# Kernel tuning notes

Hardware: AMD Instinct MI355X
Metric: run time of the kernel (lower is better)

## Reference

```python
import jax, jax.numpy as jnp
import numpy as np

N_SHAPE = 100
PARENTS = [-1, 0, 1, 1, 1]  # FLAME kintree: global, neck, jaw, eyeL, eyeR
NUM_JOINTS = 5


def batch_rodrigues(rot_vecs):
    # rot_vecs: [B, J, 3] axis-angle -> [B, J, 3, 3] rotation matrices
    angle = jnp.linalg.norm(rot_vecs + 1e-8, axis=-1, keepdims=True)  # [B,J,1]
    rot_dir = rot_vecs / angle
    cos = jnp.cos(angle)[..., None]  # [B,J,1,1]
    sin = jnp.sin(angle)[..., None]
    rx, ry, rz = rot_dir[..., 0], rot_dir[..., 1], rot_dir[..., 2]
    zeros = jnp.zeros_like(rx)
    K = jnp.stack([zeros, -rz, ry, rz, zeros, -rx, -ry, rx, zeros], axis=-1)
    K = K.reshape(rot_vecs.shape[:-1] + (3, 3))
    ident = jnp.eye(3, dtype=rot_vecs.dtype)
    return ident + sin * K + (1.0 - cos) * jnp.matmul(K, K)


def batch_rigid_transform(rot_mats, joints):
    # rot_mats: [B,J,3,3], joints: [B,J,3] -> relative transforms A: [B,J,4,4]
    B = rot_mats.shape[0]
    dtype = rot_mats.dtype
    parent_idx = jnp.array(PARENTS[1:])
    rel_joints = jnp.concatenate(
        [joints[:, :1], joints[:, 1:] - joints[:, parent_idx]], axis=1)
    # build local 4x4 transforms
    top = jnp.concatenate([rot_mats, rel_joints[..., None]], axis=-1)  # [B,J,3,4]
    bottom = jnp.broadcast_to(
        jnp.array([0.0, 0.0, 0.0, 1.0], dtype=dtype), (B, NUM_JOINTS, 1, 4))
    transforms_mat = jnp.concatenate([top, bottom], axis=-2)  # [B,J,4,4]
    # sequential FK chain over the (small, fixed) joint tree
    chain = [transforms_mat[:, 0]]
    for i in range(1, NUM_JOINTS):
        chain.append(jnp.matmul(chain[PARENTS[i]], transforms_mat[:, i]))
    transforms = jnp.stack(chain, axis=1)  # [B,J,4,4]
    # remove rest-pose joint location contribution
    joints_h = jnp.concatenate(
        [joints, jnp.zeros((B, NUM_JOINTS, 1), dtype=dtype)], axis=-1)  # [B,J,4]
    tj = jnp.matmul(transforms, joints_h[..., None])  # [B,J,4,1]
    rel_transforms = transforms - jnp.pad(tj, ((0, 0), (0, 0), (0, 0), (3, 0)))
    return rel_transforms


def _flame_forward(expression_params, full_pose, v_template, shapedirs,
                   posedirs, J_regressor, lbs_weights):
    B = expression_params.shape[0]
    V = v_template.shape[0]
    dtype = expression_params.dtype
    # betas = [zeros(n_shape) | expression]
    betas = jnp.concatenate(
        [jnp.zeros((B, N_SHAPE), dtype=dtype), expression_params], axis=1)
    # shape blendshapes
    v_shaped = v_template[None] + jnp.einsum('bl,vkl->bvk', betas, shapedirs)
    joints = jnp.einsum('jv,bvk->bjk', J_regressor, v_shaped)  # [B,J,3]
    # pose -> rotation matrices, pose feature, pose blendshapes
    rot_mats = batch_rodrigues(full_pose.reshape(B, NUM_JOINTS, 3))
    ident = jnp.eye(3, dtype=dtype)
    pose_feature = (rot_mats[:, 1:] - ident).reshape(B, (NUM_JOINTS - 1) * 9)
    pose_offsets = jnp.matmul(pose_feature, posedirs).reshape(B, V, 3)
    v_posed = v_shaped + pose_offsets
    # forward kinematics -> per-joint relative transforms
    A = batch_rigid_transform(rot_mats, joints)  # [B,J,4,4]
    # linear blend skinning
    T = jnp.einsum('vj,bjpq->bvpq', lbs_weights, A)  # [B,V,4,4]
    v_h = jnp.concatenate([v_posed, jnp.ones((B, V, 1), dtype=dtype)], axis=-1)
    verts = jnp.einsum('bvpq,bvq->bvp', T, v_h)[..., :3]
    return verts, pose_feature, A


def setup_inputs() -> dict:
    key = jax.random.key(0)
    ks = jax.random.split(key, 7)
    B, V, NE, NBASIS = 2048, 5023, 50, 150
    return {
        'expression_params': jax.random.normal(ks[0], (B, NE), jnp.float32) * 0.5,
        'full_pose': jax.random.normal(ks[1], (B, 15), jnp.float32) * 0.1,
        'v_template': jax.random.normal(ks[2], (V, 3), jnp.float32) * 0.1,
        'shapedirs': jax.random.normal(ks[3], (V, 3, NBASIS), jnp.float32) * 0.01,
        'posedirs': jax.random.normal(ks[4], (36, V * 3), jnp.float32) * 0.01,
        'J_regressor': jax.random.uniform(ks[5], (5, V), jnp.float32) / V,
        'lbs_weights': jax.nn.softmax(
            jax.random.normal(ks[6], (V, 5), jnp.float32) * 4.0, axis=-1),
    }


def reference(expression_params, full_pose, v_template, shapedirs, posedirs,
              J_regressor, lbs_weights):
    return _flame_forward(expression_params, full_pose, v_template, shapedirs,
                          posedirs, J_regressor, lbs_weights)
```

## Files before the change

kernel.cpp:

```cpp
#include <hip/hip_runtime.h>
#include <math.h>

#define NVERT 5023
#define NV3   15069
#define NEXP  50
#define NPF   36
#define NJ    5
#define BCH   128


__global__ __launch_bounds__(160) void k_jreg(const float* __restrict__ Jr,
                                              const float* __restrict__ sd,
                                              const float* __restrict__ vt,
                                              float* __restrict__ ws) {
  int t = threadIdx.x;
  int v0 = blockIdx.x * 79;
  int v1 = min(NVERT, v0 + 79);
  float acc[NJ] = {0.f, 0.f, 0.f, 0.f, 0.f};
  if (t < 150) {
    int k = t / 50, e = t - k * 50;
    const float* base = sd + k * 150 + 100 + e;
#pragma unroll 4
    for (int v = v0; v < v1; ++v) {
      float s = base[(size_t)v * 450];
#pragma unroll
      for (int j = 0; j < NJ; ++j)
        acc[j] = fmaf(Jr[j * NVERT + v], s, acc[j]);
    }
#pragma unroll
    for (int j = 0; j < NJ; ++j) atomicAdd(&ws[j * 150 + t], acc[j]);
  } else if (t < 153) {
    int k = t - 150;
#pragma unroll 4
    for (int v = v0; v < v1; ++v) {
      float s = vt[v * 3 + k];
#pragma unroll
      for (int j = 0; j < NJ; ++j)
        acc[j] = fmaf(Jr[j * NVERT + v], s, acc[j]);
    }
#pragma unroll
    for (int j = 0; j < NJ; ++j) atomicAdd(&ws[750 + j * 3 + k], acc[j]);
  }
}

__global__ __launch_bounds__(256) void k_pose(const float* __restrict__ expr,
                                              const float* __restrict__ pose,
                                              const float* __restrict__ ws,
                                              float* __restrict__ out_pf,
                                              float* __restrict__ out_A,
                                              int B) {
  int b = blockIdx.x * 256 + threadIdx.x;
  if (b >= B) return;

  float R[5][9];
#pragma unroll
  for (int j = 0; j < 5; ++j) {
    float x = pose[b * 15 + j * 3 + 0];
    float y = pose[b * 15 + j * 3 + 1];
    float z = pose[b * 15 + j * 3 + 2];
    float ax = x + 1e-8f, ay = y + 1e-8f, az = z + 1e-8f;
    float ang = sqrtf(ax * ax + ay * ay + az * az);
    float inv = 1.0f / ang;
    float ux = x * inv, uy = y * inv, uz = z * inv;
    float s = sinf(ang), c = cosf(ang), t1 = 1.0f - c;
    R[j][0] = 1.0f - t1 * (uy * uy + uz * uz);
    R[j][1] = t1 * ux * uy - s * uz;
    R[j][2] = t1 * ux * uz + s * uy;
    R[j][3] = t1 * ux * uy + s * uz;
    R[j][4] = 1.0f - t1 * (ux * ux + uz * uz);
    R[j][5] = t1 * uy * uz - s * ux;
    R[j][6] = t1 * ux * uz - s * uy;
    R[j][7] = t1 * uy * uz + s * ux;
    R[j][8] = 1.0f - t1 * (ux * ux + uy * uy);
  }

#pragma unroll
  for (int j = 1; j < 5; ++j)
#pragma unroll
    for (int i = 0; i < 9; ++i)
      out_pf[b * 36 + (j - 1) * 9 + i] =
          R[j][i] - ((i == 0 || i == 4 || i == 8) ? 1.0f : 0.0f);

  float jnt[5][3];
#pragma unroll
  for (int j = 0; j < 5; ++j)
#pragma unroll
    for (int k = 0; k < 3; ++k) jnt[j][k] = ws[750 + j * 3 + k];
  for (int e = 0; e < NEXP; ++e) {
    float ex = expr[b * NEXP + e];
#pragma unroll
    for (int j = 0; j < 5; ++j)
#pragma unroll
      for (int k = 0; k < 3; ++k)
        jnt[j][k] = fmaf(ex, ws[j * 150 + k * 50 + e], jnt[j][k]);
  }

  float* Ab = out_A + (size_t)b * 80;

  {
#pragma unroll
    for (int r = 0; r < 3; ++r) {
      float tj = R[0][r * 3 + 0] * jnt[0][0] + R[0][r * 3 + 1] * jnt[0][1] +
                 R[0][r * 3 + 2] * jnt[0][2];
      Ab[r * 4 + 0] = R[0][r * 3 + 0];
      Ab[r * 4 + 1] = R[0][r * 3 + 1];
      Ab[r * 4 + 2] = R[0][r * 3 + 2];
      Ab[r * 4 + 3] = jnt[0][r] - tj;
    }
    Ab[12] = 0.f; Ab[13] = 0.f; Ab[14] = 0.f; Ab[15] = 1.f;
  }

  float C1R[9], C1t[3];
  {
    float rel[3] = {jnt[1][0] - jnt[0][0], jnt[1][1] - jnt[0][1],
                    jnt[1][2] - jnt[0][2]};
#pragma unroll
    for (int r = 0; r < 3; ++r) {
#pragma unroll
      for (int c = 0; c < 3; ++c)
        C1R[r * 3 + c] = R[0][r * 3 + 0] * R[1][0 + c] +
                         R[0][r * 3 + 1] * R[1][3 + c] +
                         R[0][r * 3 + 2] * R[1][6 + c];
      C1t[r] = R[0][r * 3 + 0] * rel[0] + R[0][r * 3 + 1] * rel[1] +
               R[0][r * 3 + 2] * rel[2] + jnt[0][r];
    }
    float* A1 = Ab + 16;
#pragma unroll
    for (int r = 0; r < 3; ++r) {
      float tj = C1R[r * 3 + 0] * jnt[1][0] + C1R[r * 3 + 1] * jnt[1][1] +
                 C1R[r * 3 + 2] * jnt[1][2];
      A1[r * 4 + 0] = C1R[r * 3 + 0];
      A1[r * 4 + 1] = C1R[r * 3 + 1];
      A1[r * 4 + 2] = C1R[r * 3 + 2];
      A1[r * 4 + 3] = C1t[r] - tj;
    }
    A1[12] = 0.f; A1[13] = 0.f; A1[14] = 0.f; A1[15] = 1.f;
  }

#pragma unroll
  for (int i = 2; i < 5; ++i) {
    float rel[3] = {jnt[i][0] - jnt[1][0], jnt[i][1] - jnt[1][1],
                    jnt[i][2] - jnt[1][2]};
    float CiR[9], Cit[3];
#pragma unroll
    for (int r = 0; r < 3; ++r) {
#pragma unroll
      for (int c = 0; c < 3; ++c)
        CiR[r * 3 + c] = C1R[r * 3 + 0] * R[i][0 + c] +
                         C1R[r * 3 + 1] * R[i][3 + c] +
                         C1R[r * 3 + 2] * R[i][6 + c];
      Cit[r] = C1R[r * 3 + 0] * rel[0] + C1R[r * 3 + 1] * rel[1] +
               C1R[r * 3 + 2] * rel[2] + C1t[r];
    }
    float* Ai = Ab + i * 16;
#pragma unroll
    for (int r = 0; r < 3; ++r) {
      float tj = CiR[r * 3 + 0] * jnt[i][0] + CiR[r * 3 + 1] * jnt[i][1] +
                 CiR[r * 3 + 2] * jnt[i][2];
      Ai[r * 4 + 0] = CiR[r * 3 + 0];
      Ai[r * 4 + 1] = CiR[r * 3 + 1];
      Ai[r * 4 + 2] = CiR[r * 3 + 2];
      Ai[r * 4 + 3] = Cit[r] - tj;
    }
    Ai[12] = 0.f; Ai[13] = 0.f; Ai[14] = 0.f; Ai[15] = 1.f;
  }
}

__global__ __launch_bounds__(256) void k_vert(const float* __restrict__ expr,
                                              const float* __restrict__ vt,
                                              const float* __restrict__ sd,
                                              const float* __restrict__ pd,
                                              const float* __restrict__ w,
                                              const float* __restrict__ pf,
                                              const float* __restrict__ A,
                                              float* __restrict__ out, int B) {
  int wv = threadIdx.x >> 6;
  int lane = threadIdx.x & 63;
  int lvw = lane / 3;
  int kc = lane - lvw * 3;
  int v = blockIdx.x * 84 + wv * 21 + lvw;
  bool act = (lane < 63) && (v < NVERT);
  int vl = act ? v : 0;
  int srcb = lane - kc;

  float sdr[NEXP], pdr[NPF], wr[NJ];
  const float* sp = sd + (size_t)vl * 450 + kc * 150 + 100;
#pragma unroll
  for (int e = 0; e < NEXP; ++e) sdr[e] = sp[e];
#pragma unroll
  for (int p = 0; p < NPF; ++p) pdr[p] = pd[(size_t)p * NV3 + vl * 3 + kc];
#pragma unroll
  for (int j = 0; j < NJ; ++j) wr[j] = w[vl * 5 + j];
  float vtr = vt[vl * 3 + kc];

  int b0 = blockIdx.y * BCH;
  int bend = min(B, b0 + BCH);
  for (int b = b0; b < bend; ++b) {
    const float* eb = expr + (size_t)b * NEXP;
    const float* pb = pf + (size_t)b * NPF;
    const float4* A4 = (const float4*)(A + (size_t)b * 80);
    float a0 = 0.f, a1 = 0.f, a2 = 0.f, a3 = 0.f;
#pragma unroll
    for (int e = 0; e < 48; e += 4) {
      a0 = fmaf(eb[e + 0], sdr[e + 0], a0);
      a1 = fmaf(eb[e + 1], sdr[e + 1], a1);
      a2 = fmaf(eb[e + 2], sdr[e + 2], a2);
      a3 = fmaf(eb[e + 3], sdr[e + 3], a3);
    }
    a0 = fmaf(eb[48], sdr[48], a0);
    a1 = fmaf(eb[49], sdr[49], a1);
#pragma unroll
    for (int p = 0; p < 36; p += 4) {
      a0 = fmaf(pb[p + 0], pdr[p + 0], a0);
      a1 = fmaf(pb[p + 1], pdr[p + 1], a1);
      a2 = fmaf(pb[p + 2], pdr[p + 2], a2);
      a3 = fmaf(pb[p + 3], pdr[p + 3], a3);
    }
    float acc = vtr + ((a0 + a1) + (a2 + a3));
    float x0 = __shfl(acc, srcb + 0, 64);
    float x1 = __shfl(acc, srcb + 1, 64);
    float x2 = __shfl(acc, srcb + 2, 64);
    float t0 = 0.f, t1 = 0.f, t2 = 0.f, t3 = 0.f;
#pragma unroll
    for (int j = 0; j < NJ; ++j) {
      float4 aj = A4[j * 4 + kc];
      t0 = fmaf(wr[j], aj.x, t0);
      t1 = fmaf(wr[j], aj.y, t1);
      t2 = fmaf(wr[j], aj.z, t2);
      t3 = fmaf(wr[j], aj.w, t3);
    }
    float r = fmaf(t0, x0, fmaf(t1, x1, fmaf(t2, x2, t3)));
    if (act) out[(size_t)b * NV3 + (size_t)v * 3 + kc] = r;
  }
}

extern "C" void kernel_launch(void* const* d_in, const int* in_sizes, int n_in,
                              void* d_out, int out_size, void* d_ws,
                              size_t ws_size, hipStream_t stream) {
  const float* expr = (const float*)d_in[0];
  const float* pose = (const float*)d_in[1];
  const float* vt   = (const float*)d_in[2];
  const float* sd   = (const float*)d_in[3];
  const float* pd   = (const float*)d_in[4];
  const float* Jr   = (const float*)d_in[5];
  const float* w    = (const float*)d_in[6];
  int B = in_sizes[0] / NEXP;

  float* out    = (float*)d_out;
  float* out_pf = out + (size_t)B * NV3;
  float* out_A  = out_pf + (size_t)B * NPF;
  float* ws     = (float*)d_ws;

  hipMemsetAsync(d_ws, 0, 765 * sizeof(float), stream);
  k_jreg<<<dim3(64), 160, 0, stream>>>(Jr, sd, vt, ws);
  k_pose<<<(B + 255) / 256, 256, 0, stream>>>(expr, pose, ws, out_pf, out_A, B);
  k_vert<<<dim3((NVERT + 83) / 84, (B + BCH - 1) / BCH), 256, 0, stream>>>(
      expr, vt, sd, pd, w, out_pf, out_A, out, B);
}
```

Before: 399.1 us.

## Rewrite vertex kernel as shared-memory tiled GEMM and restructure joint regression

The per-vertex kernel becomes a 64-batch by 120-column tiled GEMM over the 86 combined expression and pose coefficients, staged in shared memory with register-blocked accumulation, followed by a skinning pass that reads the A transforms from shared memory. Joint regression drops atomics in favour of per-block partial sums plus a separate reduction kernel. The pose kernel stages its outputs in shared memory for coalesced stores and switches to fast __sinf/__cosf. The goal is to cut the redundant per-batch global reads of expr, pf and A, at the cost of an extra launch and some precision loss in the trig functions.

```diff
diff --git a/kernel.cpp b/kernel.cpp
--- a/kernel.cpp
+++ b/kernel.cpp
@@ -6,32 +6,49 @@
 #define NEXP  50
 #define NPF   36
 #define NJ    5
-#define BCH   128
-
+
+#define JBLK 126
+#define JCH  40
+#define PSTR 800
+#define WSJ  (JBLK * PSTR)
 
 __global__ __launch_bounds__(160) void k_jreg(const float* __restrict__ Jr,
                                               const float* __restrict__ sd,
                                               const float* __restrict__ vt,
                                               float* __restrict__ ws) {
   int t = threadIdx.x;
-  int v0 = blockIdx.x * 79;
-  int v1 = min(NVERT, v0 + 79);
+  if (t >= 153) return;
+  int v0 = blockIdx.x * JCH;
+  int v1 = min(NVERT, v0 + JCH);
   float acc[NJ] = {0.f, 0.f, 0.f, 0.f, 0.f};
+  float* pb = ws + blockIdx.x * PSTR;
   if (t < 150) {
     int k = t / 50, e = t - k * 50;
     const float* base = sd + k * 150 + 100 + e;
-#pragma unroll 4
-    for (int v = v0; v < v1; ++v) {
+    int v = v0;
+    for (; v + 4 <= v1; v += 4) {
+      float s0 = base[(size_t)(v + 0) * 450];
+      float s1 = base[(size_t)(v + 1) * 450];
+      float s2 = base[(size_t)(v + 2) * 450];
+      float s3 = base[(size_t)(v + 3) * 450];
+#pragma unroll
+      for (int j = 0; j < NJ; ++j) {
+        acc[j] = fmaf(Jr[j * NVERT + v + 0], s0, acc[j]);
+        acc[j] = fmaf(Jr[j * NVERT + v + 1], s1, acc[j]);
+        acc[j] = fmaf(Jr[j * NVERT + v + 2], s2, acc[j]);
+        acc[j] = fmaf(Jr[j * NVERT + v + 3], s3, acc[j]);
+      }
+    }
+    for (; v < v1; ++v) {
       float s = base[(size_t)v * 450];
 #pragma unroll
       for (int j = 0; j < NJ; ++j)
         acc[j] = fmaf(Jr[j * NVERT + v], s, acc[j]);
     }
 #pragma unroll
-    for (int j = 0; j < NJ; ++j) atomicAdd(&ws[j * 150 + t], acc[j]);
-  } else if (t < 153) {
+    for (int j = 0; j < NJ; ++j) pb[j * 160 + t] = acc[j];
+  } else {
     int k = t - 150;
-#pragma unroll 4
     for (int v = v0; v < v1; ++v) {
       float s = vt[v * 3 + k];
 #pragma unroll
@@ -39,65 +56,79 @@
         acc[j] = fmaf(Jr[j * NVERT + v], s, acc[j]);
     }
 #pragma unroll
-    for (int j = 0; j < NJ; ++j) atomicAdd(&ws[750 + j * 3 + k], acc[j]);
-  }
-}
-
-__global__ __launch_bounds__(256) void k_pose(const float* __restrict__ expr,
-                                              const float* __restrict__ pose,
-                                              const float* __restrict__ ws,
-                                              float* __restrict__ out_pf,
-                                              float* __restrict__ out_A,
-                                              int B) {
-  int b = blockIdx.x * 256 + threadIdx.x;
-  if (b >= B) return;
-
-  float R[5][9];
-#pragma unroll
-  for (int j = 0; j < 5; ++j) {
-    float x = pose[b * 15 + j * 3 + 0];
-    float y = pose[b * 15 + j * 3 + 1];
-    float z = pose[b * 15 + j * 3 + 2];
-    float ax = x + 1e-8f, ay = y + 1e-8f, az = z + 1e-8f;
-    float ang = sqrtf(ax * ax + ay * ay + az * az);
-    float inv = 1.0f / ang;
-    float ux = x * inv, uy = y * inv, uz = z * inv;
-    float s = sinf(ang), c = cosf(ang), t1 = 1.0f - c;
-    R[j][0] = 1.0f - t1 * (uy * uy + uz * uz);
-    R[j][1] = t1 * ux * uy - s * uz;
-    R[j][2] = t1 * ux * uz + s * uy;
-    R[j][3] = t1 * ux * uy + s * uz;
-    R[j][4] = 1.0f - t1 * (ux * ux + uz * uz);
-    R[j][5] = t1 * uy * uz - s * ux;
-    R[j][6] = t1 * ux * uz - s * uy;
-    R[j][7] = t1 * uy * uz + s * ux;
-    R[j][8] = 1.0f - t1 * (ux * ux + uy * uy);
-  }
-
-#pragma unroll
-  for (int j = 1; j < 5; ++j)
-#pragma unroll
-    for (int i = 0; i < 9; ++i)
-      out_pf[b * 36 + (j - 1) * 9 + i] =
-          R[j][i] - ((i == 0 || i == 4 || i == 8) ? 1.0f : 0.0f);
-
-  float jnt[5][3];
-#pragma unroll
-  for (int j = 0; j < 5; ++j)
-#pragma unroll
-    for (int k = 0; k < 3; ++k) jnt[j][k] = ws[750 + j * 3 + k];
-  for (int e = 0; e < NEXP; ++e) {
-    float ex = expr[b * NEXP + e];
+    for (int j = 0; j < NJ; ++j) pb[j * 160 + 150 + k] = acc[j];
+  }
+}
+
+__global__ __launch_bounds__(256) void k_jred(float* __restrict__ ws) {
+  int o = blockIdx.x * 256 + threadIdx.x;
+  if (o >= 765) return;
+  int j = o / 153, t = o - j * 153;
+  int off = j * 160 + t;
+  float s = 0.f;
+#pragma unroll 6
+  for (int bk = 0; bk < JBLK; ++bk) s += ws[bk * PSTR + off];
+  ws[WSJ + off] = s;
+}
+
+__global__ __launch_bounds__(64) void k_pose(const float* __restrict__ expr,
+                                             const float* __restrict__ pose,
+                                             const float* __restrict__ ws,
+                                             float* __restrict__ out_pf,
+                                             float* __restrict__ out_A,
+                                             int B) {
+  __shared__ float pf_s[64 * 36];
+  __shared__ float A_s[64 * 80];
+  int t = threadIdx.x;
+  int b0 = blockIdx.x * 64;
+  int b = b0 + t;
+  const float* wsJ = ws + WSJ;
+
+  if (b < B) {
+    float R[5][9];
+#pragma unroll
+    for (int j = 0; j < 5; ++j) {
+      float x = pose[b * 15 + j * 3 + 0];
+      float y = pose[b * 15 + j * 3 + 1];
+      float z = pose[b * 15 + j * 3 + 2];
+      float ax = x + 1e-8f, ay = y + 1e-8f, az = z + 1e-8f;
+      float ang = sqrtf(ax * ax + ay * ay + az * az);
+      float inv = 1.0f / ang;
+      float ux = x * inv, uy = y * inv, uz = z * inv;
+      float s = __sinf(ang), c = __cosf(ang), t1 = 1.0f - c;
+      R[j][0] = 1.0f - t1 * (uy * uy + uz * uz);
+      R[j][1] = t1 * ux * uy - s * uz;
+      R[j][2] = t1 * ux * uz + s * uy;
+      R[j][3] = t1 * ux * uy + s * uz;
+      R[j][4] = 1.0f - t1 * (ux * ux + uz * uz);
+      R[j][5] = t1 * uy * uz - s * ux;
+      R[j][6] = t1 * ux * uz - s * uy;
+      R[j][7] = t1 * uy * uz + s * ux;
+      R[j][8] = 1.0f - t1 * (ux * ux + uy * uy);
+    }
+
+#pragma unroll
+    for (int j = 1; j < 5; ++j)
+#pragma unroll
+      for (int i = 0; i < 9; ++i)
+        pf_s[t * 36 + (j - 1) * 9 + i] =
+            R[j][i] - ((i == 0 || i == 4 || i == 8) ? 1.0f : 0.0f);
+
+    float jnt[5][3];
 #pragma unroll
     for (int j = 0; j < 5; ++j)
 #pragma unroll
-      for (int k = 0; k < 3; ++k)
-        jnt[j][k] = fmaf(ex, ws[j * 150 + k * 50 + e], jnt[j][k]);
-  }
-
-  float* Ab = out_A + (size_t)b * 80;
-
-  {
+      for (int k = 0; k < 3; ++k) jnt[j][k] = wsJ[j * 160 + 150 + k];
+    for (int e = 0; e < NEXP; ++e) {
+      float ex = expr[b * NEXP + e];
+#pragma unroll
+      for (int j = 0; j < 5; ++j)
+#pragma unroll
+        for (int k = 0; k < 3; ++k)
+          jnt[j][k] = fmaf(ex, wsJ[j * 160 + k * 50 + e], jnt[j][k]);
+    }
+
+    float* Ab = A_s + t * 80;
 #pragma unroll
     for (int r = 0; r < 3; ++r) {
       float tj = R[0][r * 3 + 0] * jnt[0][0] + R[0][r * 3 + 1] * jnt[0][1] +
@@ -108,64 +139,74 @@
       Ab[r * 4 + 3] = jnt[0][r] - tj;
     }
     Ab[12] = 0.f; Ab[13] = 0.f; Ab[14] = 0.f; Ab[15] = 1.f;
-  }
-
-  float C1R[9], C1t[3];
-  {
-    float rel[3] = {jnt[1][0] - jnt[0][0], jnt[1][1] - jnt[0][1],
-                    jnt[1][2] - jnt[0][2]};
-#pragma unroll
-    for (int r = 0; r < 3; ++r) {
-#pragma unroll
-      for (int c = 0; c < 3; ++c)
-        C1R[r * 3 + c] = R[0][r * 3 + 0] * R[1][0 + c] +
-                         R[0][r * 3 + 1] * R[1][3 + c] +
-                         R[0][r * 3 + 2] * R[1][6 + c];
-      C1t[r] = R[0][r * 3 + 0] * rel[0] + R[0][r * 3 + 1] * rel[1] +
-               R[0][r * 3 + 2] * rel[2] + jnt[0][r];
-    }
-    float* A1 = Ab + 16;
-#pragma unroll
-    for (int r = 0; r < 3; ++r) {
-      float tj = C1R[r * 3 + 0] * jnt[1][0] + C1R[r * 3 + 1] * jnt[1][1] +
-                 C1R[r * 3 + 2] * jnt[1][2];
-      A1[r * 4 + 0] = C1R[r * 3 + 0];
-      A1[r * 4 + 1] = C1R[r * 3 + 1];
-      A1[r * 4 + 2] = C1R[r * 3 + 2];
-      A1[r * 4 + 3] = C1t[r] - tj;
-    }
-    A1[12] = 0.f; A1[13] = 0.f; A1[14] = 0.f; A1[15] = 1.f;
-  }
-
-#pragma unroll
-  for (int i = 2; i < 5; ++i) {
-    float rel[3] = {jnt[i][0] - jnt[1][0], jnt[i][1] - jnt[1][1],
-                    jnt[i][2] - jnt[1][2]};
-    float CiR[9], Cit[3];
-#pragma unroll
-    for (int r = 0; r < 3; ++r) {
-#pragma unroll
-      for (int c = 0; c < 3; ++c)
-        CiR[r * 3 + c] = C1R[r * 3 + 0] * R[i][0 + c] +
-                         C1R[r * 3 + 1] * R[i][3 + c] +
-                         C1R[r * 3 + 2] * R[i][6 + c];
-      Cit[r] = C1R[r * 3 + 0] * rel[0] + C1R[r * 3 + 1] * rel[1] +
-               C1R[r * 3 + 2] * rel[2] + C1t[r];
-    }
-    float* Ai = Ab + i * 16;
-#pragma unroll
-    for (int r = 0; r < 3; ++r) {
-      float tj = CiR[r * 3 + 0] * jnt[i][0] + CiR[r * 3 + 1] * jnt[i][1] +
-                 CiR[r * 3 + 2] * jnt[i][2];
-      Ai[r * 4 + 0] = CiR[r * 3 + 0];
-      Ai[r * 4 + 1] = CiR[r * 3 + 1];
-      Ai[r * 4 + 2] = CiR[r * 3 + 2];
-      Ai[r * 4 + 3] = Cit[r] - tj;
-    }
-    Ai[12] = 0.f; Ai[13] = 0.f; Ai[14] = 0.f; Ai[15] = 1.f;
-  }
-}
-
+
+    float C1R[9], C1t[3];
+    {
+      float rel[3] = {jnt[1][0] - jnt[0][0], jnt[1][1] - jnt[0][1],
+                      jnt[1][2] - jnt[0][2]};
+#pragma unroll
+      for (int r = 0; r < 3; ++r) {
+#pragma unroll
+        for (int c = 0; c < 3; ++c)
+          C1R[r * 3 + c] = R[0][r * 3 + 0] * R[1][0 + c] +
+                           R[0][r * 3 + 1] * R[1][3 + c] +
+                           R[0][r * 3 + 2] * R[1][6 + c];
+        C1t[r] = R[0][r * 3 + 0] * rel[0] + R[0][r * 3 + 1] * rel[1] +
+                 R[0][r * 3 + 2] * rel[2] + jnt[0][r];
+      }
+      float* A1 = Ab + 16;
+#pragma unroll
+      for (int r = 0; r < 3; ++r) {
+        float tj = C1R[r * 3 + 0] * jnt[1][0] + C1R[r * 3 + 1] * jnt[1][1] +
+                   C1R[r * 3 + 2] * jnt[1][2];
+        A1[r * 4 + 0] = C1R[r * 3 + 0];
+        A1[r * 4 + 1] = C1R[r * 3 + 1];
+        A1[r * 4 + 2] = C1R[r * 3 + 2];
+        A1[r * 4 + 3] = C1t[r] - tj;
+      }
+      A1[12] = 0.f; A1[13] = 0.f; A1[14] = 0.f; A1[15] = 1.f;
+    }
+
+#pragma unroll
+    for (int i = 2; i < 5; ++i) {
+      float rel[3] = {jnt[i][0] - jnt[1][0], jnt[i][1] - jnt[1][1],
+                      jnt[i][2] - jnt[1][2]};
+      float CiR[9], Cit[3];
+#pragma unroll
+      for (int r = 0; r < 3; ++r) {
+#pragma unroll
+        for (int c = 0; c < 3; ++c)
+          CiR[r * 3 + c] = C1R[r * 3 + 0] * R[i][0 + c] +
+                           C1R[r * 3 + 1] * R[i][3 + c] +
+                           C1R[r * 3 + 2] * R[i][6 + c];
+        Cit[r] = C1R[r * 3 + 0] * rel[0] + C1R[r * 3 + 1] * rel[1] +
+                 C1R[r * 3 + 2] * rel[2] + C1t[r];
+      }
+      float* Ai = Ab + i * 16;
+#pragma unroll
+      for (int r = 0; r < 3; ++r) {
+        float tj = CiR[r * 3 + 0] * jnt[i][0] + CiR[r * 3 + 1] * jnt[i][1] +
+                   CiR[r * 3 + 2] * jnt[i][2];
+        Ai[r * 4 + 0] = CiR[r * 3 + 0];
+        Ai[r * 4 + 1] = CiR[r * 3 + 1];
+        Ai[r * 4 + 2] = CiR[r * 3 + 2];
+        Ai[r * 4 + 3] = Cit[r] - tj;
+      }
+      Ai[12] = 0.f; Ai[13] = 0.f; Ai[14] = 0.f; Ai[15] = 1.f;
+    }
+  }
+  __syncthreads();
+  for (int r = 0; r < 36; ++r)
+    out_pf[(size_t)b0 * 36 + r * 64 + t] = pf_s[r * 64 + t];
+  for (int r = 0; r < 80; ++r)
+    out_A[(size_t)b0 * 80 + r * 64 + t] = A_s[r * 64 + t];
+}
+
+#define BM 64
+#define BN 120
+#define KK 86
+#define GSTR 68
+#define CSTR 124
 __global__ __launch_bounds__(256) void k_vert(const float* __restrict__ expr,
                                               const float* __restrict__ vt,
                                               const float* __restrict__ sd,
@@ -174,63 +215,103 @@
                                               const float* __restrict__ pf,
                                               const float* __restrict__ A,
                                               float* __restrict__ out, int B) {
-  int wv = threadIdx.x >> 6;
-  int lane = threadIdx.x & 63;
-  int lvw = lane / 3;
-  int kc = lane - lvw * 3;
-  int v = blockIdx.x * 84 + wv * 21 + lvw;
-  bool act = (lane < 63) && (v < NVERT);
-  int vl = act ? v : 0;
-  int srcb = lane - kc;
-
-  float sdr[NEXP], pdr[NPF], wr[NJ];
-  const float* sp = sd + (size_t)vl * 450 + kc * 150 + 100;
-#pragma unroll
-  for (int e = 0; e < NEXP; ++e) sdr[e] = sp[e];
-#pragma unroll
-  for (int p = 0; p < NPF; ++p) pdr[p] = pd[(size_t)p * NV3 + vl * 3 + kc];
-#pragma unroll
-  for (int j = 0; j < NJ; ++j) wr[j] = w[vl * 5 + j];
-  float vtr = vt[vl * 3 + kc];
-
-  int b0 = blockIdx.y * BCH;
-  int bend = min(B, b0 + BCH);
-  for (int b = b0; b < bend; ++b) {
-    const float* eb = expr + (size_t)b * NEXP;
-    const float* pb = pf + (size_t)b * NPF;
-    const float4* A4 = (const float4*)(A + (size_t)b * 80);
-    float a0 = 0.f, a1 = 0.f, a2 = 0.f, a3 = 0.f;
-#pragma unroll
-    for (int e = 0; e < 48; e += 4) {
-      a0 = fmaf(eb[e + 0], sdr[e + 0], a0);
-      a1 = fmaf(eb[e + 1], sdr[e + 1], a1);
-      a2 = fmaf(eb[e + 2], sdr[e + 2], a2);
-      a3 = fmaf(eb[e + 3], sdr[e + 3], a3);
-    }
-    a0 = fmaf(eb[48], sdr[48], a0);
-    a1 = fmaf(eb[49], sdr[49], a1);
-#pragma unroll
-    for (int p = 0; p < 36; p += 4) {
-      a0 = fmaf(pb[p + 0], pdr[p + 0], a0);
-      a1 = fmaf(pb[p + 1], pdr[p + 1], a1);
-      a2 = fmaf(pb[p + 2], pdr[p + 2], a2);
-      a3 = fmaf(pb[p + 3], pdr[p + 3], a3);
-    }
-    float acc = vtr + ((a0 + a1) + (a2 + a3));
-    float x0 = __shfl(acc, srcb + 0, 64);
-    float x1 = __shfl(acc, srcb + 1, 64);
-    float x2 = __shfl(acc, srcb + 2, 64);
-    float t0 = 0.f, t1 = 0.f, t2 = 0.f, t3 = 0.f;
-#pragma unroll
-    for (int j = 0; j < NJ; ++j) {
-      float4 aj = A4[j * 4 + kc];
-      t0 = fmaf(wr[j], aj.x, t0);
-      t1 = fmaf(wr[j], aj.y, t1);
-      t2 = fmaf(wr[j], aj.z, t2);
-      t3 = fmaf(wr[j], aj.w, t3);
-    }
-    float r = fmaf(t0, x0, fmaf(t1, x1, fmaf(t2, x2, t3)));
-    if (act) out[(size_t)b * NV3 + (size_t)v * 3 + kc] = r;
+  __shared__ float Gs[KK * GSTR];
+  __shared__ float Ss[KK * BN + 8];
+  int tid = threadIdx.x;
+  int tx = tid & 15;
+  int ty = tid >> 4;
+  int i0 = blockIdx.x * BN;
+  int b0 = blockIdx.y * BM;
+  int vbase = i0 / 3;
+
+  for (int idx = tid; idx < 22 * BN; idx += 256) {
+    int rq = idx / BN, col = idx - rq * BN;
+    int ig = min(i0 + col, NV3 - 1);
+    int v = ig / 3, kc = ig - 3 * v;
+#pragma unroll
+    for (int q = 0; q < 4; ++q) {
+      int r = rq * 4 + q;
+      if (r < KK) {
+        float val = (r < 50) ? sd[(size_t)v * 450 + kc * 150 + 100 + r]
+                             : pd[(size_t)(r - 50) * NV3 + ig];
+        Ss[r * BN + col] = val;
+      }
+    }
+  }
+  for (int idx = tid; idx < KK * BM; idx += 256) {
+    int k = idx >> 6, bb = idx & 63;
+    float val = (k < 50) ? expr[(size_t)(b0 + bb) * 50 + k]
+                         : pf[(size_t)(b0 + bb) * 36 + (k - 50)];
+    Gs[k * GSTR + bb] = val;
+  }
+  float vtv[8];
+#pragma unroll
+  for (int n = 0; n < 8; ++n)
+    vtv[n] = vt[min(i0 + 8 * tx + n, NV3 - 1)];
+  float acc[4][8];
+#pragma unroll
+  for (int m = 0; m < 4; ++m)
+#pragma unroll
+    for (int n = 0; n < 8; ++n) acc[m][n] = vtv[n];
+  __syncthreads();
+
+#pragma unroll 2
+  for (int k = 0; k < KK; ++k) {
+    float4 g  = *(const float4*)&Gs[k * GSTR + 4 * ty];
+    float4 s0 = *(const float4*)&Ss[k * BN + 8 * tx];
+    float4 s1 = *(const float4*)&Ss[k * BN + 8 * tx + 4];
+    float gm[4] = {g.x, g.y, g.z, g.w};
+    float sn[8] = {s0.x, s0.y, s0.z, s0.w, s1.x, s1.y, s1.z, s1.w};
+#pragma unroll
+    for (int m = 0; m < 4; ++m)
+#pragma unroll
+      for (int n = 0; n < 8; ++n)
+        acc[m][n] = fmaf(gm[m], sn[n], acc[m][n]);
+  }
+  __syncthreads();
+
+  if (tx < 15) {
+#pragma unroll
+    for (int m = 0; m < 4; ++m) {
+      float4 c0 = {acc[m][0], acc[m][1], acc[m][2], acc[m][3]};
+      float4 c1 = {acc[m][4], acc[m][5], acc[m][6], acc[m][7]};
+      *(float4*)&Ss[(4 * ty + m) * CSTR + 8 * tx]     = c0;
+      *(float4*)&Ss[(4 * ty + m) * CSTR + 8 * tx + 4] = c1;
+    }
+  }
+  for (int idx = tid; idx < BM * 80; idx += 256)
+    Gs[idx] = A[(size_t)b0 * 80 + idx];
+  __syncthreads();
+
+  int nv = min(40, NVERT - vbase);
+#pragma unroll
+  for (int p = 0; p < 10; ++p) {
+    int P = tid + p * 256;
+    int v = P % 40, bb = P / 40;
+    if (v >= nv) continue;
+    const float* wp = w + (size_t)(vbase + v) * 5;
+    float w0 = wp[0], w1 = wp[1], w2 = wp[2], w3 = wp[3], w4 = wp[4];
+    const float* Ab = Gs + bb * 80;
+    float T[12];
+#pragma unroll
+    for (int rc = 0; rc < 12; ++rc) T[rc] = w0 * Ab[rc];
+#pragma unroll
+    for (int rc = 0; rc < 12; ++rc) T[rc] = fmaf(w1, Ab[16 + rc], T[rc]);
+#pragma unroll
+    for (int rc = 0; rc < 12; ++rc) T[rc] = fmaf(w2, Ab[32 + rc], T[rc]);
+#pragma unroll
+    for (int rc = 0; rc < 12; ++rc) T[rc] = fmaf(w3, Ab[48 + rc], T[rc]);
+#pragma unroll
+    for (int rc = 0; rc < 12; ++rc) T[rc] = fmaf(w4, Ab[64 + rc], T[rc]);
+    float x0 = Ss[bb * CSTR + 3 * v + 0];
+    float x1 = Ss[bb * CSTR + 3 * v + 1];
+    float x2 = Ss[bb * CSTR + 3 * v + 2];
+    size_t ob = (size_t)(b0 + bb) * NV3 + i0 + 3 * v;
+#pragma unroll
+    for (int q = 0; q < 3; ++q)
+      out[ob + q] = fmaf(T[q * 4 + 0], x0,
+                    fmaf(T[q * 4 + 1], x1,
+                    fmaf(T[q * 4 + 2], x2, T[q * 4 + 3])));
   }
 }
 
@@ -251,9 +332,10 @@
   float* out_A  = out_pf + (size_t)B * NPF;
   float* ws     = (float*)d_ws;
 
-  hipMemsetAsync(d_ws, 0, 765 * sizeof(float), stream);
-  k_jreg<<<dim3(64), 160, 0, stream>>>(Jr, sd, vt, ws);
-  k_pose<<<(B + 255) / 256, 256, 0, stream>>>(expr, pose, ws, out_pf, out_A, B);
-  k_vert<<<dim3((NVERT + 83) / 84, (B + BCH - 1) / BCH), 256, 0, stream>>>(
+  k_jreg<<<dim3(JBLK), 160, 0, stream>>>(Jr, sd, vt, ws);
+  k_jred<<<dim3(3), 256, 0, stream>>>(ws);
+  k_pose<<<dim3((B + 63) / 64), 64, 0, stream>>>(expr, pose, ws, out_pf,
+                                                 out_A, B);
+  k_vert<<<dim3((NV3 + BN - 1) / BN, (B + BM - 1) / BM), 256, 0, stream>>>(
       expr, vt, sd, pd, w, out_pf, out_A, out, B);
 }
```

Measured after the change: 390.5 us. -2.2%, faster.
